# Optimization experiments

Measured on AMD Instinct MI355X. Metric: run time of the kernel, lower is better.

The kernel has to match this reference:

```python
import jax, jax.numpy as jnp
import numpy as np

# TT decomposition config (from Eff_TTEmbedding args in source)
P = (216, 216, 216)      # auto-factorized p_shapes for n=10,000,000 (216^3 >= n)
Q = (2, 4, 2)            # tt_q_shapes, prod = 16 = embedding_dim
R = (128, 128)           # tt_ranks
NUM_TABLES = 2
BATCH = 1024
NUM_EMB = 10_000_000


def setup_inputs() -> dict:
    key = jax.random.key(0)
    k0, k1, k2, k3 = jax.random.split(key, 4)
    # sparse indices per TT table: [n_tables, batch]
    lS_i = jax.random.randint(k3, (NUM_TABLES, BATCH), 0, NUM_EMB, dtype=jnp.int64)
    # TT cores, weight_dist='uniform'
    core0 = jax.random.uniform(k0, (NUM_TABLES, P[0], Q[0] * R[0]), dtype=jnp.float32, minval=-0.01, maxval=0.01)
    core1 = jax.random.uniform(k1, (NUM_TABLES, P[1], R[0] * Q[1] * R[1]), dtype=jnp.float32, minval=-0.01, maxval=0.01)
    core2 = jax.random.uniform(k2, (NUM_TABLES, P[2], R[1] * Q[2]), dtype=jnp.float32, minval=-0.01, maxval=0.01)
    return {"lS_i": lS_i, "core0": core0, "core1": core1, "core2": core2}


def _tt_lookup(idx, c0, c1, c2):
    """TT embedding lookup for one table. idx: [B] int; returns [B, prod(Q)]."""
    B = idx.shape[0]
    # mixed-radix decomposition of flat index into (i0, i1, i2)
    i0 = idx // (P[1] * P[2])
    i1 = (idx // P[2]) % P[1]
    i2 = idx % P[2]
    # gather TT core slices (the memory-bound irregular access)
    A = c0[i0].reshape(B, Q[0], R[0])            # [B, 2, 128]
    Bm = c1[i1].reshape(B, R[0], Q[1] * R[1])    # [B, 128, 512]
    C = c2[i2].reshape(B, R[1], Q[2])            # [B, 128, 2]
    # chained small matmuls along TT ranks
    AB = jnp.einsum('bqr,brs->bqs', A, Bm).reshape(B, Q[0] * Q[1], R[1])  # [B, 8, 128]
    out = jnp.einsum('bqr,brs->bqs', AB, C)      # [B, 8, 2]
    return out.reshape(B, Q[0] * Q[1] * Q[2])    # [B, 16]


def reference(lS_i, core0, core1, core2):
    # per-table dispatch (forward returns one embedding bag per TT table)
    return jax.vmap(_tt_lookup)(lS_i, core0, core1, core2)  # [n_tables, B, 16]
```

## Files before the change

kernel.cpp:

```cpp
#include <hip/hip_runtime.h>


#define NGROUPS 432
#define NLOOK   2048

__global__ __launch_bounds__(512) void tt_prep(const int* __restrict__ idx32,
                                               int* __restrict__ w) {
    __shared__ int cnt[NGROUPS];
    __shared__ int wtot[8];
    __shared__ int cursor[NGROUPS];
    const int tid  = threadIdx.x;
    const int lane = tid & 63;
    const int wv   = tid >> 6;

    for (int i = tid; i < NGROUPS; i += 512) cnt[i] = 0;
    __syncthreads();

    const bool is64 = (idx32[1] == 0) & (idx32[3] == 0) &
                      (idx32[5] == 0) & (idx32[7] == 0);

    int grp[4];
#pragma unroll
    for (int j = 0; j < 4; ++j) {
        const int id = tid + j * 512;
        const unsigned idx = is64 ? (unsigned)((const long long*)idx32)[id]
                                  : (unsigned)idx32[id];
        const unsigned i0  = idx / 46656u;
        const unsigned rem = idx - i0 * 46656u;
        const unsigned i1  = rem / 216u;
        const unsigned i2  = rem - i1 * 216u;
        const int table = id >> 10;
        grp[j] = table * 216 + (int)i1;
        w[2912 + id] = (int)((i0 << 16) | i2);
        atomicAdd(&cnt[grp[j]], 1);
    }
    __syncthreads();

    const int v = (tid < NGROUPS) ? cnt[tid] : 0;
    int s = v;
#pragma unroll
    for (int d = 1; d < 64; d <<= 1) {
        const int t = __shfl_up(s, d);
        if (lane >= d) s += t;
    }
    if (lane == 63) wtot[wv] = s;
    __syncthreads();
    int off = 0;
    for (int i = 0; i < wv; ++i) off += wtot[i];
    if (tid < NGROUPS) {
        const int st = s + off - v;
        w[tid]       = st;
        w[432 + tid] = v;
        cursor[tid]  = st;
    }
    __syncthreads();

#pragma unroll
    for (int j = 0; j < 4; ++j) {
        const int id  = tid + j * 512;
        const int pos = atomicAdd(&cursor[grp[j]], 1);
        w[864 + pos] = id;
    }
}

__global__ __launch_bounds__(128) void tt_main(
    const float* __restrict__ c0,
    const float* __restrict__ c1,
    const float* __restrict__ c2,
    const int* __restrict__ w,
    float* __restrict__ out)
{
    const int g  = blockIdx.x;
    const int q  = blockIdx.y;
    const int cs = blockIdx.z;
    const int m = w[432 + g];
    if (m <= cs * 8) return;
    const int s0    = w[g];
    const int table = g / 216;
    const int i1    = g - table * 216;

    const int tid = threadIdx.x;
    const int rh  = tid >> 6;
    const int tl  = tid & 63;

    __shared__ float lds[2048];
    float2* lds2 = (float2*)lds;
    __shared__ int s_id[8];
    __shared__ int s_aux[8];

    const float2* b2 = (const float2*)(c1 + (((size_t)(table * 216 + i1)) << 16))
                       + (size_t)rh * 64 * 256 + (q * 64 + tl);
    const float* c0t = c0 + (size_t)table * 216 * 256;

    for (int base = cs * 8; base < m; base += 16) {
        const int cl = min(8, m - base);
        __syncthreads();
        if (tid < 8) {
            const bool ok = tid < cl;
            const int id  = ok ? w[864 + s0 + base + tid] : 0;
            s_id[tid]  = id;
            s_aux[tid] = ok ? w[2912 + id] : 0;
        }
        __syncthreads();

#pragma unroll
        for (int l = 0; l < 8; ++l) {
            const float* ar = c0t + (size_t)(s_aux[l] >> 16) * 256;
#pragma unroll
            for (int k = 0; k < 2; ++k) {
                const int e = tid + 128 * k;
                lds[l * 256 + 2 * (e & 127) + (e >> 7)] = ar[e];
            }
        }
        __syncthreads();

        float2 acc[8][2];
#pragma unroll
        for (int l = 0; l < 8; ++l) {
            acc[l][0] = make_float2(0.f, 0.f);
            acc[l][1] = make_float2(0.f, 0.f);
        }

#pragma unroll 8
        for (int rr = 0; rr < 64; ++rr) {
            const float2 bv = b2[(size_t)rr * 256];
            const int r = rh * 64 + rr;
#pragma unroll
            for (int l = 0; l < 8; ++l) {
                const float2 av = lds2[l * 128 + r];
                acc[l][0].x += av.x * bv.x; acc[l][0].y += av.x * bv.y;
                acc[l][1].x += av.y * bv.x; acc[l][1].y += av.y * bv.y;
            }
        }

        __syncthreads();
        if (rh == 1) {
#pragma unroll
            for (int l = 0; l < 8; ++l) {
                lds2[(l * 2 + 0) * 64 + tl] = acc[l][0];
                lds2[(l * 2 + 1) * 64 + tl] = acc[l][1];
            }
        }
        __syncthreads();

        if (rh == 0) {
#pragma unroll
            for (int l = 0; l < 8; ++l) {
                const float2 t0 = lds2[(l * 2 + 0) * 64 + tl];
                const float2 t1 = lds2[(l * 2 + 1) * 64 + tl];
                const float a0x = acc[l][0].x + t0.x, a0y = acc[l][0].y + t0.y;
                const float a1x = acc[l][1].x + t1.x, a1y = acc[l][1].y + t1.y;
                if (l < cl) {
                    const float* crow = c2 + (size_t)(table * 216 + (s_aux[l] & 0xffff)) * 256;
                    const float4 cv = *(const float4*)(crow + 4 * tl);
                    float p00 = a0x * cv.x + a0y * cv.z;
                    float p01 = a0x * cv.y + a0y * cv.w;
                    float p10 = a1x * cv.x + a1y * cv.z;
                    float p11 = a1x * cv.y + a1y * cv.w;
#pragma unroll
                    for (int mm = 32; mm >= 1; mm >>= 1) {
                        p00 += __shfl_xor(p00, mm);
                        p01 += __shfl_xor(p01, mm);
                        p10 += __shfl_xor(p10, mm);
                        p11 += __shfl_xor(p11, mm);
                    }
                    if (tl == 0) {
                        float* o = out + (size_t)s_id[l] * 16;
                        o[q * 2 + 0]     = p00;
                        o[q * 2 + 1]     = p01;
                        o[8 + q * 2 + 0] = p10;
                        o[8 + q * 2 + 1] = p11;
                    }
                }
            }
        }
    }
}

extern "C" void kernel_launch(void* const* d_in, const int* in_sizes, int n_in,
                              void* d_out, int out_size, void* d_ws, size_t ws_size,
                              hipStream_t stream) {
    const int*   idx = (const int*)d_in[0];
    const float* c0  = (const float*)d_in[1];
    const float* c1  = (const float*)d_in[2];
    const float* c2  = (const float*)d_in[3];
    float* out = (float*)d_out;
    int* w = (int*)d_ws;

    tt_prep<<<dim3(1), dim3(512), 0, stream>>>(idx, w);
    tt_main<<<dim3(NGROUPS, 4, 2), dim3(128), 0, stream>>>(c0, c1, c2, w, out);
}
```

Measured before the change: 182.2 us.

## Fuse index bucketing into main kernel, drop separate prep launch

Removes the single-block prep kernel. Each (group, q) block now scans its table's 1024 indices itself and collects the matching i1 entries into shared memory with an atomic counter, capped at CAP=128. The grid loses the z-split over chunks, the rank loop is restructured to read float4 from LDS covering two ranks at once, and the epilogue now spreads across both wavefronts instead of only one. The aim is to drop a serialized launch and workspace round-trip. In exchange every block redundantly decodes 1024 indices, and groups holding more than 128 lookups would silently drop entries.

```diff
diff --git a/kernel.cpp b/kernel.cpp
--- a/kernel.cpp
+++ b/kernel.cpp
@@ -1,81 +1,17 @@
 #include <hip/hip_runtime.h>
 
 
-#define NGROUPS 432
-#define NLOOK   2048
+#define CAP 128
 
-__global__ __launch_bounds__(512) void tt_prep(const int* __restrict__ idx32,
-                                               int* __restrict__ w) {
-    __shared__ int cnt[NGROUPS];
-    __shared__ int wtot[8];
-    __shared__ int cursor[NGROUPS];
-    const int tid  = threadIdx.x;
-    const int lane = tid & 63;
-    const int wv   = tid >> 6;
-
-    for (int i = tid; i < NGROUPS; i += 512) cnt[i] = 0;
-    __syncthreads();
-
-    const bool is64 = (idx32[1] == 0) & (idx32[3] == 0) &
-                      (idx32[5] == 0) & (idx32[7] == 0);
-
-    int grp[4];
-#pragma unroll
-    for (int j = 0; j < 4; ++j) {
-        const int id = tid + j * 512;
-        const unsigned idx = is64 ? (unsigned)((const long long*)idx32)[id]
-                                  : (unsigned)idx32[id];
-        const unsigned i0  = idx / 46656u;
-        const unsigned rem = idx - i0 * 46656u;
-        const unsigned i1  = rem / 216u;
-        const unsigned i2  = rem - i1 * 216u;
-        const int table = id >> 10;
-        grp[j] = table * 216 + (int)i1;
-        w[2912 + id] = (int)((i0 << 16) | i2);
-        atomicAdd(&cnt[grp[j]], 1);
-    }
-    __syncthreads();
-
-    const int v = (tid < NGROUPS) ? cnt[tid] : 0;
-    int s = v;
-#pragma unroll
-    for (int d = 1; d < 64; d <<= 1) {
-        const int t = __shfl_up(s, d);
-        if (lane >= d) s += t;
-    }
-    if (lane == 63) wtot[wv] = s;
-    __syncthreads();
-    int off = 0;
-    for (int i = 0; i < wv; ++i) off += wtot[i];
-    if (tid < NGROUPS) {
-        const int st = s + off - v;
-        w[tid]       = st;
-        w[432 + tid] = v;
-        cursor[tid]  = st;
-    }
-    __syncthreads();
-
-#pragma unroll
-    for (int j = 0; j < 4; ++j) {
-        const int id  = tid + j * 512;
-        const int pos = atomicAdd(&cursor[grp[j]], 1);
-        w[864 + pos] = id;
-    }
-}
-
-__global__ __launch_bounds__(128) void tt_main(
+__global__ __launch_bounds__(128) void tt_fused(
+    const int* __restrict__ idx32,
     const float* __restrict__ c0,
     const float* __restrict__ c1,
     const float* __restrict__ c2,
-    const int* __restrict__ w,
     float* __restrict__ out)
 {
-    const int g  = blockIdx.x;
-    const int q  = blockIdx.y;
-    const int cs = blockIdx.z;
-    const int m = w[432 + g];
-    if (m <= cs * 8) return;
-    const int s0    = w[g];
+    const int g     = blockIdx.x;
+    const int q     = blockIdx.y;
     const int table = g / 216;
     const int i1    = g - table * 216;
 
@@ -83,29 +19,50 @@
     const int rh  = tid >> 6;
     const int tl  = tid & 63;
 
-    __shared__ float lds[2048];
-    float2* lds2 = (float2*)lds;
-    __shared__ int s_id[8];
-    __shared__ int s_aux[8];
+    __shared__ float lds[4096];
+    __shared__ int s_id[CAP];
+    __shared__ int s_aux[CAP];
+    __shared__ int s_cnt;
 
-    const float2* b2 = (const float2*)(c1 + (((size_t)(table * 216 + i1)) << 16))
+    if (tid == 0) s_cnt = 0;
+    __syncthreads();
+
+    const bool is64 = (idx32[1] == 0) & (idx32[3] == 0) &
+                      (idx32[5] == 0) & (idx32[7] == 0);
+
+    for (int j = tid; j < 1024; j += 128) {
+        const int id = (table << 10) + j;
+        const unsigned idx = is64 ? (unsigned)((const long long*)idx32)[id]
+                                  : (unsigned)idx32[id];
+        const unsigned i0  = idx / 46656u;
+        const unsigned rem = idx - i0 * 46656u;
+        const unsigned bi1 = rem / 216u;
+        if ((int)bi1 == i1) {
+            const unsigned i2 = rem - bi1 * 216u;
+            const int pos = atomicAdd(&s_cnt, 1);
+            if (pos < CAP) {
+                s_id[pos]  = id;
+                s_aux[pos] = (int)((i0 << 16) | i2);
+            }
+        }
+    }
+    __syncthreads();
+    const int m = min(s_cnt, CAP);
+    if (m == 0) return;
+
+    float2*       lds2 = (float2*)lds;
+    const float4* lds4 = (const float4*)lds;
+
+    const float2* b2 = (const float2*)(c1 + ((size_t)g << 16))
                        + (size_t)rh * 64 * 256 + (q * 64 + tl);
     const float* c0t = c0 + (size_t)table * 216 * 256;
 
-    for (int base = cs * 8; base < m; base += 16) {
+    for (int base = 0; base < m; base += 8) {
         const int cl = min(8, m - base);
         __syncthreads();
-        if (tid < 8) {
-            const bool ok = tid < cl;
-            const int id  = ok ? w[864 + s0 + base + tid] : 0;
-            s_id[tid]  = id;
-            s_aux[tid] = ok ? w[2912 + id] : 0;
-        }
-        __syncthreads();
 
-#pragma unroll
-        for (int l = 0; l < 8; ++l) {
-            const float* ar = c0t + (size_t)(s_aux[l] >> 16) * 256;
+        for (int l = 0; l < cl; ++l) {
+            const float* ar = c0t + (size_t)(s_aux[base + l] >> 16) * 256;
 #pragma unroll
             for (int k = 0; k < 2; ++k) {
                 const int e = tid + 128 * k;
@@ -122,55 +79,55 @@
         }
 
 #pragma unroll 8
-        for (int rr = 0; rr < 64; ++rr) {
-            const float2 bv = b2[(size_t)rr * 256];
-            const int r = rh * 64 + rr;
+        for (int rr2 = 0; rr2 < 32; ++rr2) {
+            const float2 bv0 = b2[(size_t)(2 * rr2) * 256];
+            const float2 bv1 = b2[(size_t)(2 * rr2 + 1) * 256];
+            const int rhalf = rh * 32 + rr2;
 #pragma unroll
             for (int l = 0; l < 8; ++l) {
-                const float2 av = lds2[l * 128 + r];
-                acc[l][0].x += av.x * bv.x; acc[l][0].y += av.x * bv.y;
-                acc[l][1].x += av.y * bv.x; acc[l][1].y += av.y * bv.y;
+                const float4 av = lds4[l * 64 + rhalf];
+                acc[l][0].x += av.x * bv0.x; acc[l][0].y += av.x * bv0.y;
+                acc[l][1].x += av.y * bv0.x; acc[l][1].y += av.y * bv0.y;
+                acc[l][0].x += av.z * bv1.x; acc[l][0].y += av.z * bv1.y;
+                acc[l][1].x += av.w * bv1.x; acc[l][1].y += av.w * bv1.y;
             }
         }
 
         __syncthreads();
-        if (rh == 1) {
 #pragma unroll
-            for (int l = 0; l < 8; ++l) {
-                lds2[(l * 2 + 0) * 64 + tl] = acc[l][0];
-                lds2[(l * 2 + 1) * 64 + tl] = acc[l][1];
-            }
+        for (int l = 0; l < 8; ++l) {
+            lds2[((rh * 8 + l) * 2 + 0) * 64 + tl] = acc[l][0];
+            lds2[((rh * 8 + l) * 2 + 1) * 64 + tl] = acc[l][1];
         }
         __syncthreads();
 
-        if (rh == 0) {
 #pragma unroll
-            for (int l = 0; l < 8; ++l) {
-                const float2 t0 = lds2[(l * 2 + 0) * 64 + tl];
-                const float2 t1 = lds2[(l * 2 + 1) * 64 + tl];
-                const float a0x = acc[l][0].x + t0.x, a0y = acc[l][0].y + t0.y;
-                const float a1x = acc[l][1].x + t1.x, a1y = acc[l][1].y + t1.y;
-                if (l < cl) {
-                    const float* crow = c2 + (size_t)(table * 216 + (s_aux[l] & 0xffff)) * 256;
-                    const float4 cv = *(const float4*)(crow + 4 * tl);
-                    float p00 = a0x * cv.x + a0y * cv.z;
-                    float p01 = a0x * cv.y + a0y * cv.w;
-                    float p10 = a1x * cv.x + a1y * cv.z;
-                    float p11 = a1x * cv.y + a1y * cv.w;
+        for (int ll = 0; ll < 4; ++ll) {
+            const int l = 2 * ll + rh;
+            if (l < cl) {
+                const float2 u0 = lds2[((0 * 8 + l) * 2 + 0) * 64 + tl];
+                const float2 u1 = lds2[((1 * 8 + l) * 2 + 0) * 64 + tl];
+                const float2 v0 = lds2[((0 * 8 + l) * 2 + 1) * 64 + tl];
+                const float2 v1 = lds2[((1 * 8 + l) * 2 + 1) * 64 + tl];
+                const float a0x = u0.x + u1.x, a0y = u0.y + u1.y;
+                const float a1x = v0.x + v1.x, a1y = v0.y + v1.y;
+                const float* crow = c2 + (size_t)(table * 216 + (s_aux[base + l] & 0xffff)) * 256;
+                const float4 cv = *(const float4*)(crow + 4 * tl);
+                float p00 = a0x * cv.x + a0y * cv.z;
+                float p01 = a0x * cv.y + a0y * cv.w;
+                float p10 = a1x * cv.x + a1y * cv.z;
+                float p11 = a1x * cv.y + a1y * cv.w;
 #pragma unroll
-                    for (int mm = 32; mm >= 1; mm >>= 1) {
-                        p00 += __shfl_xor(p00, mm);
-                        p01 += __shfl_xor(p01, mm);
-                        p10 += __shfl_xor(p10, mm);
-                        p11 += __shfl_xor(p11, mm);
-                    }
-                    if (tl == 0) {
-                        float* o = out + (size_t)s_id[l] * 16;
-                        o[q * 2 + 0]     = p00;
-                        o[q * 2 + 1]     = p01;
-                        o[8 + q * 2 + 0] = p10;
-                        o[8 + q * 2 + 1] = p11;
-                    }
+                for (int mm = 32; mm >= 1; mm >>= 1) {
+                    p00 += __shfl_xor(p00, mm);
+                    p01 += __shfl_xor(p01, mm);
+                    p10 += __shfl_xor(p10, mm);
+                    p11 += __shfl_xor(p11, mm);
+                }
+                if (tl == 0) {
+                    float* o = out + (size_t)s_id[base + l] * 16;
+                    *(float2*)(o + q * 2)     = make_float2(p00, p01);
+                    *(float2*)(o + 8 + q * 2) = make_float2(p10, p11);
                 }
             }
         }
@@ -185,8 +142,7 @@
     const float* c1  = (const float*)d_in[2];
     const float* c2  = (const float*)d_in[3];
     float* out = (float*)d_out;
-    int* w = (int*)d_ws;
+    (void)d_ws; (void)ws_size; (void)in_sizes; (void)n_in; (void)out_size;
 
-    tt_prep<<<dim3(1), dim3(512), 0, stream>>>(idx, w);
-    tt_main<<<dim3(NGROUPS, 4, 2), dim3(128), 0, stream>>>(c0, c1, c2, w, out);
+    tt_fused<<<dim3(432, 4), dim3(128), 0, stream>>>(idx, c0, c1, c2, out);
 }
```

Result: slower. 194.0 us (+6.5%).
